# Kernel optimization log

Hardware: AMD Instinct MI355X
Metric: run time of the kernel (lower is better)

Reference implementation:

```python
import jax, jax.numpy as jnp
from jax import lax
import numpy as np

B, T, F = 256, 256, 40
H, A, HORIZON = 256, 64, 60
D_SP = 192


def setup_inputs() -> dict:
    key = jax.random.key(0)
    ks = jax.random.split(key, 16)
    s = 0.05  # weight scale to keep activations stable
    return {
        'x': jax.random.normal(ks[0], (B, T, F), jnp.float32),
        'W_sp': jax.random.normal(ks[1], (F, D_SP), jnp.float32) * s,
        'b_sp': jnp.zeros((D_SP,), jnp.float32),
        'Wx_ef': jax.random.normal(ks[2], (D_SP, 4 * H), jnp.float32) * s,
        'Wh_ef': jax.random.normal(ks[3], (H, 4 * H), jnp.float32) * s,
        'b_ef': jnp.zeros((4 * H,), jnp.float32),
        'Wx_eb': jax.random.normal(ks[4], (D_SP, 4 * H), jnp.float32) * s,
        'Wh_eb': jax.random.normal(ks[5], (H, 4 * H), jnp.float32) * s,
        'b_eb': jnp.zeros((4 * H,), jnp.float32),
        'We': jax.random.normal(ks[6], (2 * H, A), jnp.float32) * s,
        'Wd': jax.random.normal(ks[7], (H, A), jnp.float32) * s,
        'v': jax.random.normal(ks[8], (A,), jnp.float32) * s,
        'Wx_d': jax.random.normal(ks[9], (1 + 2 * H, 4 * H), jnp.float32) * s,
        'Wh_d': jax.random.normal(ks[10], (H, 4 * H), jnp.float32) * s,
        'b_d': jnp.zeros((4 * H,), jnp.float32),
        'W_ih': jax.random.normal(ks[11], (2 * H, H), jnp.float32) * s,
        'b_ih': jnp.zeros((H,), jnp.float32),
        'W_ic': jax.random.normal(ks[12], (2 * H, H), jnp.float32) * s,
        'b_ic': jnp.zeros((H,), jnp.float32),
        'Wo': jax.random.normal(ks[13], (H, 1), jnp.float32) * s,
        'bo': jnp.zeros((1,), jnp.float32),
    }


def _lstm_cell(x_t, h, c, Wx, Wh, b):
    g = x_t @ Wx + h @ Wh + b
    i, f, gg, o = jnp.split(g, 4, axis=-1)  # torch gate order i,f,g,o
    c = jax.nn.sigmoid(f) * c + jax.nn.sigmoid(i) * jnp.tanh(gg)
    h = jax.nn.sigmoid(o) * jnp.tanh(c)
    return h, c


def _lstm_scan(xs_tbd, Wx, Wh, b):
    # xs_tbd: [T, B, D] -> hs [T, B, H]
    h0 = jnp.zeros((xs_tbd.shape[1], Wh.shape[0]), xs_tbd.dtype)
    c0 = jnp.zeros_like(h0)
    def step(carry, x_t):
        h, c = carry
        h, c = _lstm_cell(x_t, h, c, Wx, Wh, b)
        return (h, c), h
    _, hs = lax.scan(step, (h0, c0), xs_tbd)
    return hs


def reference(x, W_sp, b_sp, Wx_ef, Wh_ef, b_ef, Wx_eb, Wh_eb, b_eb,
              We, Wd, v, Wx_d, Wh_d, b_d, W_ih, b_ih, W_ic, b_ic, Wo, bo):
    # spatial encoder (stand-in for DeepLOBEncoder): [B,T,F] -> [B,T,192]
    h_spatial = x @ W_sp + b_sp
    xs = jnp.swapaxes(h_spatial, 0, 1)          # [T, B, 192]
    hs_f = _lstm_scan(xs, Wx_ef, Wh_ef, b_ef)    # [T, B, H]
    hs_b = _lstm_scan(xs[::-1], Wx_eb, Wh_eb, b_eb)[::-1]
    enc_out = jnp.swapaxes(jnp.concatenate([hs_f, hs_b], axis=-1), 0, 1)  # [B,T,2H]

    enc_mean = enc_out.mean(axis=1)
    dec_h = jnp.tanh(enc_mean @ W_ih + b_ih)     # [B, H]
    dec_c = jnp.tanh(enc_mean @ W_ic + b_ic)

    enc_proj = enc_out @ We                      # [B, T, A] precomputed (same math)
    prev_y = ((x[:, -1, 0] + x[:, -1, 2]) / 2.0)[:, None]  # ask_idx=0, bid_idx=2

    def dec_step(carry, _):
        h, c, py = carry
        e = jnp.tanh(enc_proj + (h @ Wd)[:, None, :])        # [B,T,A]
        scores = e @ v                                        # [B,T]
        w = jax.nn.softmax(scores, axis=1)
        context = jnp.einsum('bt,bth->bh', w, enc_out)        # [B,2H]
        dec_in = jnp.concatenate([py, context], axis=1)       # [B,1+2H]
        h, c = _lstm_cell(dec_in, h, c, Wx_d, Wh_d, b_d)
        y = h @ Wo + bo                                       # [B,1]
        return (h, c, lax.stop_gradient(y)), y[:, 0]

    _, ys = lax.scan(dec_step, (dec_h, dec_c, prev_y), None, length=HORIZON)
    return jnp.swapaxes(ys, 0, 1)  # [B, horizon]
```

## Files before the change

kernel.cpp:

```cpp
#include <hip/hip_runtime.h>
#include <cmath>

#define B_ 256
#define T_ 256
#define F_ 40
#define H_ 256
#define A_ 64
#define HOR_ 60
#define DSP_ 192
#define ENC_NBLK 128
#define WSTR 456
#define FPAD 32
#define ADLD 1024
#define CT 56

typedef unsigned short u16;
typedef unsigned int u32;
typedef __attribute__((ext_vector_type(8))) short bf16x8;
typedef __attribute__((ext_vector_type(4))) float f32x4;
typedef __attribute__((ext_vector_type(8))) u32 u32x8;
typedef __attribute__((ext_vector_type(4))) u32 u32x4;

__device__ __forceinline__ float sigm(float x){ return 1.f/(1.f+expf(-x)); }

__device__ __forceinline__ u16 f2bf(float x){
  u32 u = __float_as_uint(x);
  u32 r = (u + 0x7FFFu + ((u>>16)&1u)) >> 16;
  return (u16)r;
}
__device__ __forceinline__ float bf2f(u16 h){ return __uint_as_float(((u32)h)<<16); }
__device__ __forceinline__ u32 packsplit(float x){
  u16 hi = f2bf(x);
  u16 lo = f2bf(x - bf2f(hi));
  return (u32)hi | ((u32)lo<<16);
}
__device__ __forceinline__ float unpack2f(u32 v){
  return __uint_as_float(v<<16) + __uint_as_float(v & 0xFFFF0000u);
}

__device__ __forceinline__ float wred_sum(float v){
  #pragma unroll
  for (int o=32;o>0;o>>=1) v += __shfl_xor(v,o);
  return v;
}
__device__ __forceinline__ float wred_max(float v){
  #pragma unroll
  for (int o=32;o>0;o>>=1) v = fmaxf(v,__shfl_xor(v,o));
  return v;
}

__device__ __forceinline__ void cnt_signal(int* c){
  __hip_atomic_fetch_add(c, 1, __ATOMIC_RELEASE, __HIP_MEMORY_SCOPE_AGENT);
}
template<int SLP>
__device__ __forceinline__ void cnt_wait4(const int* base, int need, int tid){
  if (tid < 4){
    const int* c = base + (size_t)tid*FPAD;
    while (__hip_atomic_load(c, __ATOMIC_ACQUIRE, __HIP_MEMORY_SCOPE_AGENT) < need)
      __builtin_amdgcn_s_sleep(SLP);
  }
  __syncthreads();
}

__global__ void conv_w(const float* __restrict__ Wx, const float* __restrict__ Wh,
                       u16* __restrict__ hi, u16* __restrict__ lo,
                       int KX, int Ktot, int N){
  int idx = blockIdx.x*256 + threadIdx.x;
  if (idx >= N*Ktot) return;
  int n = idx / Ktot, k = idx - n*Ktot;
  float w = (k < KX) ? Wx[(size_t)k*N + n] : Wh[(size_t)(k-KX)*N + n];
  u16 h = f2bf(w);
  hi[idx] = h;
  lo[idx] = f2bf(w - bf2f(h));
}

__global__ __launch_bounds__(192) void spatial_proj(
    const float* __restrict__ x, const float* __restrict__ W, const float* __restrict__ bsp,
    u32* __restrict__ hsp32){
  __shared__ float Ws[40][192];
  __shared__ float xr[40];
  int t = blockIdx.x, tid = threadIdx.x;
  for (int i = tid; i < 40*192; i += 192){ int k = i/192, c = i-k*192; Ws[k][c] = W[i]; }
  float bb = bsp[tid];
  __syncthreads();
  for (int b=0; b<B_; b++){
    if (tid < 40) xr[tid] = x[((size_t)b*T_ + t)*F_ + tid];
    __syncthreads();
    float acc = bb;
    #pragma unroll
    for (int k=0;k<40;k++) acc += xr[k]*Ws[k][tid];
    hsp32[((size_t)t*B_ + b)*DSP_ + tid] = packsplit(acc);
    __syncthreads();
  }
}

__global__ __launch_bounds__(256) void enc_scan(
    const u32* __restrict__ hsp32,
    const u16* __restrict__ W_hi, const u16* __restrict__ W_lo,
    const float* __restrict__ b_ef, const float* __restrict__ b_eb,
    u32* __restrict__ hbuf, u32* __restrict__ eo32, int* __restrict__ bar)
{
  extern __shared__ u16 smem[];
  u16* Whi = smem;
  u16* Wlo = smem + 4*16*WSTR;
  const int bid = blockIdx.x;
  const int grp = bid & 7;
  const int nt  = bid >> 3;
  const int dir = grp >> 2;
  const int m0  = (grp & 3) * 64;
  const int u0  = nt * 16;
  const int tid = threadIdx.x;
  const int wave = tid >> 6, lane = tid & 63;
  const int lrow = lane & 15, kblk = lane >> 4;
  const int koff = kblk * 8;
  {
    const size_t wbase = ((size_t)dir*1024 + u0) * 448;
    for (int idx = tid; idx < 4*16*448; idx += 256){
      int g = idx / (16*448);
      int r = idx - g*(16*448);
      int j = r / 448;
      int k = r - j*448;
      size_t go = wbase + ((size_t)g*256 + j)*448 + k;
      Whi[(g*16 + j)*WSTR + k] = W_hi[go];
      Wlo[(g*16 + j)*WSTR + k] = W_lo[go];
    }
  }
  const float* bias = dir ? b_eb : b_ef;
  float bg4[4];
  #pragma unroll
  for (int g=0; g<4; g++) bg4[g] = bias[g*H_ + u0 + lrow];
  __syncthreads();

  const int mrow = m0 + wave*16;
  const int arow = mrow + lrow;
  u32* hP0 = hbuf + (size_t)dir*(B_*H_);
  u32* hP1 = hbuf + (size_t)(2+dir)*(B_*H_);
  float c_reg[4] = {0.f,0.f,0.f,0.f};

  for (int s=0; s<T_; s++){
    const int t = dir ? (T_-1-s) : s;
    f32x4 acc[4] = {};
    const u32* abase = hsp32 + ((size_t)t*B_ + arow)*DSP_;
    #pragma unroll
    for (int ks=0; ks<6; ks++){
      int kb = ks*32 + koff;
      u32x8 la = *(const u32x8*)(abase + kb);
      bf16x8 ah, al;
      #pragma unroll
      for (int j=0;j<8;j++){ ah[j]=(short)(la[j]&0xFFFFu); al[j]=(short)(la[j]>>16); }
      #pragma unroll
      for (int g=0; g<4; g++){
        bf16x8 bh = *(const bf16x8*)(Whi + (g*16+lrow)*WSTR + kb);
        bf16x8 bl = *(const bf16x8*)(Wlo + (g*16+lrow)*WSTR + kb);
        acc[g] = __builtin_amdgcn_mfma_f32_16x16x32_bf16(ah, bh, acc[g], 0,0,0);
        acc[g] = __builtin_amdgcn_mfma_f32_16x16x32_bf16(ah, bl, acc[g], 0,0,0);
        acc[g] = __builtin_amdgcn_mfma_f32_16x16x32_bf16(al, bh, acc[g], 0,0,0);
      }
    }
    if (s > 0)
      cnt_wait4<8>(bar + (size_t)((grp*T_ + (s-1))*4)*FPAD, 4, tid);
    const u32* hin = (s & 1) ? hP1 : hP0;
    u32* hout      = (s & 1) ? hP0 : hP1;
    const u32* hbase = hin + (size_t)arow*H_;
    #pragma unroll
    for (int ks=0; ks<8; ks++){
      int kb = ks*32 + koff;
      u32x8 la = *(const u32x8*)(hbase + kb);
      bf16x8 ah, al;
      #pragma unroll
      for (int j=0;j<8;j++){ ah[j]=(short)(la[j]&0xFFFFu); al[j]=(short)(la[j]>>16); }
      #pragma unroll
      for (int g=0; g<4; g++){
        bf16x8 bh = *(const bf16x8*)(Whi + (g*16+lrow)*WSTR + 192 + kb);
        bf16x8 bl = *(const bf16x8*)(Wlo + (g*16+lrow)*WSTR + 192 + kb);
        acc[g] = __builtin_amdgcn_mfma_f32_16x16x32_bf16(ah, bh, acc[g], 0,0,0);
        acc[g] = __builtin_amdgcn_mfma_f32_16x16x32_bf16(ah, bl, acc[g], 0,0,0);
        acc[g] = __builtin_amdgcn_mfma_f32_16x16x32_bf16(al, bh, acc[g], 0,0,0);
      }
    }
    #pragma unroll
    for (int r=0; r<4; r++){
      int brow = mrow + kblk*4 + r;
      float gi = acc[0][r] + bg4[0];
      float gf = acc[1][r] + bg4[1];
      float gg = acc[2][r] + bg4[2];
      float go = acc[3][r] + bg4[3];
      float cn = sigm(gf)*c_reg[r] + sigm(gi)*tanhf(gg);
      float hn = sigm(go)*tanhf(cn);
      c_reg[r] = cn;
      u32 hp = packsplit(hn);
      hout[(size_t)brow*H_ + u0 + lrow] = hp;
      eo32[((size_t)brow*T_ + t)*512 + dir*H_ + u0 + lrow] = hp;
    }
    if (s == T_-1) break;
    __syncthreads();
    if (tid == 0)
      cnt_signal(bar + (size_t)((grp*T_ + s)*4 + (nt>>2))*FPAD);
  }
}

__global__ __launch_bounds__(512) void dec_scan(
    const u32* __restrict__ eo32,
    const u16* __restrict__ Wet_hi, const u16* __restrict__ Wet_lo,
    const float* __restrict__ W_ih, const float* __restrict__ b_ih,
    const float* __restrict__ W_ic, const float* __restrict__ b_ic,
    const float* __restrict__ x, float* __restrict__ ep,
    const float* __restrict__ Wd, const float* __restrict__ v,
    const float* __restrict__ Wo, const float* __restrict__ bo,
    const u16* __restrict__ W_hi, const u16* __restrict__ W_lo,
    const float* __restrict__ b_d, const float* __restrict__ Wx_d,
    float* __restrict__ hdp, float* __restrict__ cd,
    u32* __restrict__ Ad32, float* __restrict__ py,
    float* __restrict__ out, int* __restrict__ cntA, int* __restrict__ cntB)
{
  __shared__ float sh_h[256], sh_hwd[64], sh_v[64], sh_sc[256], sh_w[256];
  __shared__ float red8[8][64];
  __shared__ float sh_red[4], sh_red2[4];
  __shared__ float redc[8][512];
  __shared__ float gl[8][16][16];
  __shared__ float em_s[512];
  __shared__ u32 eoL[CT*512];
  const int b = blockIdx.x, tid = threadIdx.x;
  const int wave = tid >> 6, lane = tid & 63;
  const int bx = ((b & 7) << 1) | ((b >> 3) & 1);
  const int by = b >> 4;
  const int cr = tid >> 4, cu = tid & 15;
  float c_reg = 0.f;
  float bg0=0,bg1=0,bg2=0,bg3=0, w00=0,w01=0,w02=0,w03=0;
  if (tid < 256){
    int uu = bx*16 + cu;
    bg0 = b_d[uu];       bg1 = b_d[256+uu];
    bg2 = b_d[512+uu];   bg3 = b_d[768+uu];
    w00 = Wx_d[uu];      w01 = Wx_d[256+uu];
    w02 = Wx_d[512+uu];  w03 = Wx_d[768+uu];
  }
  {
    const u32* src = eo32 + (size_t)b*T_*512;
    for (int i = tid; i < CT*512/4; i += 512)
      ((u32x4*)eoL)[i] = *(const u32x4*)(src + (size_t)i*4);
  }
  {
    const int lrow = lane & 15, kblk = lane >> 4, koff = kblk*8;
    #pragma unroll
    for (int mi=0; mi<2; mi++){
      int mt = wave*2 + mi;
      f32x4 acc[4] = {};
      for (int ks=0; ks<16; ks++){
        int kb = ks*32 + koff;
        u32x8 ld = *(const u32x8*)(eo32 + ((size_t)b*T_ + mt*16 + lrow)*512 + kb);
        bf16x8 ah, al;
        #pragma unroll
        for (int j=0;j<8;j++){ ah[j]=(short)(ld[j]&0xFFFFu); al[j]=(short)(ld[j]>>16); }
        #pragma unroll
        for (int nf=0; nf<4; nf++){
          bf16x8 bh = *(const bf16x8*)(Wet_hi + (size_t)(nf*16+lrow)*512 + kb);
          bf16x8 bl = *(const bf16x8*)(Wet_lo + (size_t)(nf*16+lrow)*512 + kb);
          acc[nf] = __builtin_amdgcn_mfma_f32_16x16x32_bf16(ah, bh, acc[nf], 0,0,0);
          acc[nf] = __builtin_amdgcn_mfma_f32_16x16x32_bf16(ah, bl, acc[nf], 0,0,0);
          acc[nf] = __builtin_amdgcn_mfma_f32_16x16x32_bf16(al, bh, acc[nf], 0,0,0);
        }
      }
      #pragma unroll
      for (int nf=0; nf<4; nf++)
        #pragma unroll
        for (int r=0; r<4; r++)
          ep[((size_t)b*T_ + mt*16 + kblk*4 + r)*64 + nf*16 + lrow] = acc[nf][r];
    }
  }
  {
    float cacc[8] = {};
    const u32* eo = eo32 + (size_t)b*T_*512 + lane*8;
    #pragma unroll 8
    for (int tt=0; tt<32; tt++){
      int t = wave*32 + tt;
      u32x4 e0 = *(const u32x4*)(eo + (size_t)t*512);
      u32x4 e1 = *(const u32x4*)(eo + (size_t)t*512 + 4);
      #pragma unroll
      for (int j=0;j<4;j++){ cacc[j] += unpack2f(e0[j]); cacc[4+j] += unpack2f(e1[j]); }
    }
    #pragma unroll
    for (int j=0;j<8;j++) redc[wave][lane*8+j] = cacc[j];
    __syncthreads();
    if (tid < 256){
      float s0=0.f, s1=0.f;
      #pragma unroll
      for (int q=0;q<8;q++){ s0 += redc[q][tid]; s1 += redc[q][256+tid]; }
      em_s[tid] = s0*(1.f/T_); em_s[256+tid] = s1*(1.f/T_);
    }
    __syncthreads();
  }
  if (tid < 256){
    float ah = b_ih[tid], ac = b_ic[tid];
    for (int k=0;k<512;k++){
      float e = em_s[k];
      ah += e*W_ih[(size_t)k*256 + tid];
      ac += e*W_ic[(size_t)k*256 + tid];
    }
    float h0 = tanhf(ah), c0 = tanhf(ac);
    sh_h[tid] = h0;
    hdp[(size_t)b*H_ + tid] = h0;
    Ad32[(size_t)b*ADLD + 512 + tid] = packsplit(h0);
    cd[(size_t)b*H_ + tid] = c0;
  }
  if (tid == 0){
    size_t xb = ((size_t)b*T_ + 255)*F_;
    py[b] = (x[xb] + x[xb+2])*0.5f;
  }
  if (tid >= 448) sh_v[tid-448] = v[tid-448];
  __syncthreads();
  for (int s=0; s<=HOR_; s++){
    if (s > 0){
      cnt_wait4<16>(cntB + (size_t)(((s-1)*16 + by)*4)*FPAD, 4, tid);
      if (tid < 256) sh_h[tid] = hdp[(size_t)(s&1)*B_*H_ + (size_t)b*H_ + tid];
      __syncthreads();
      if (tid < 256){
        float p = sh_h[tid] * Wo[tid];
        p = wred_sum(p);
        if ((tid & 63) == 0) sh_red[tid>>6] = p;
      }
      __syncthreads();
      if (tid == 0){
        float y = sh_red[0]+sh_red[1]+sh_red[2]+sh_red[3] + bo[0];
        out[b*HOR_ + (s-1)] = y;
        py[b] = y;
      }
    }
    if (s == HOR_) break;
    {
      float ssum = 0.f;
      for (int j=wave*32; j<wave*32+32; j++) ssum += sh_h[j]*Wd[(size_t)j*A_ + lane];
      red8[wave][lane] = ssum;
      __syncthreads();
      if (tid < 64){
        float a = 0.f;
        #pragma unroll
        for (int q=0;q<8;q++) a += red8[q][tid];
        sh_hwd[tid] = a;
      }
    }
    __syncthreads();
    {
      int t = tid >> 1, aa = tid & 1;
      const float4* ep4 = (const float4*)(ep + ((size_t)(b*T_+t))*A_ + aa*32);
      float partial = 0.f;
      #pragma unroll
      for (int q=0;q<8;q++){
        float4 e4 = ep4[q];
        int a0 = aa*32 + q*4;
        partial += tanhf(e4.x + sh_hwd[a0+0]) * sh_v[a0+0];
        partial += tanhf(e4.y + sh_hwd[a0+1]) * sh_v[a0+1];
        partial += tanhf(e4.z + sh_hwd[a0+2]) * sh_v[a0+2];
        partial += tanhf(e4.w + sh_hwd[a0+3]) * sh_v[a0+3];
      }
      partial += __shfl_xor(partial, 1);
      if (aa == 0) sh_sc[t] = partial;
    }
    __syncthreads();
    if (tid < 256){
      float sc = sh_sc[tid];
      float m = wred_max(sc);
      if ((tid&63)==0) sh_red[tid>>6] = m;
      __syncthreads();
      m = fmaxf(fmaxf(sh_red[0],sh_red[1]), fmaxf(sh_red[2],sh_red[3]));
      float e = expf(sc - m);
      float su = wred_sum(e);
      if ((tid&63)==0) sh_red2[tid>>6] = su;
      __syncthreads();
      su = (sh_red2[0]+sh_red2[1])+(sh_red2[2]+sh_red2[3]);
      sh_w[tid] = e / su;
    } else { __syncthreads(); __syncthreads(); }
    __syncthreads();
    {
      float cacc[8] = {};
      const int t0 = wave*32, t1 = t0 + 32;
      const int tL = (t1 < CT) ? t1 : CT;
      for (int t=t0; t<tL; ++t){
        float wgt = sh_w[t];
        const u32* p = eoL + t*512 + lane*8;
        u32x4 e0 = *(const u32x4*)p;
        u32x4 e1 = *(const u32x4*)(p + 4);
        #pragma unroll
        for (int j=0;j<4;j++){
          cacc[j]   += wgt * unpack2f(e0[j]);
          cacc[4+j] += wgt * unpack2f(e1[j]);
        }
      }
      const u32* eo = eo32 + (size_t)b*T_*512 + lane*8;
      const int tG = (t0 > CT) ? t0 : CT;
      #pragma unroll 8
      for (int t=tG; t<t1; ++t){
        float wgt = sh_w[t];
        u32x4 e0 = *(const u32x4*)(eo + (size_t)t*512);
        u32x4 e1 = *(const u32x4*)(eo + (size_t)t*512 + 4);
        #pragma unroll
        for (int j=0;j<4;j++){
          cacc[j]   += wgt * unpack2f(e0[j]);
          cacc[4+j] += wgt * unpack2f(e1[j]);
        }
      }
      #pragma unroll
      for (int j=0;j<8;j++) redc[wave][lane*8+j] = cacc[j];
    }
    __syncthreads();
    if (tid < 256){
      float c0 = 0.f, c1 = 0.f;
      #pragma unroll
      for (int q=0;q<8;q++){ c0 += redc[q][tid]; c1 += redc[q][256+tid]; }
      Ad32[(size_t)b*ADLD + tid]       = packsplit(c0);
      Ad32[(size_t)b*ADLD + 256 + tid] = packsplit(c1);
    }
    __syncthreads();
    if (tid == 0)
      cnt_signal(cntA + (size_t)((s*16 + (b>>4))*4 + ((b&15)>>2))*FPAD);
    const int par = s & 1;
    const int gB = wave & 3, khB = wave >> 2;
    const int r16 = lane & 15, kb4 = lane >> 4;
    f32x4 accB = {0.f,0.f,0.f,0.f};
    const u32* arB = Ad32 + (size_t)(by*16 + r16)*ADLD;
    const u16* WHB = W_hi + (size_t)(gB*256 + bx*16 + r16)*768;
    const u16* WLB = W_lo + (size_t)(gB*256 + bx*16 + r16)*768;
    const bool pre = (khB == 1) && (s > 0);
    if (pre){
      for (int ks=16; ks<24; ks++){
        int kb = ks*32 + kb4*8;
        int kp = kb + (par<<8);
        u32x8 ld = *(const u32x8*)(arB + kp);
        bf16x8 ah, al;
        #pragma unroll
        for (int j=0;j<8;j++){ ah[j]=(short)(ld[j]&0xFFFFu); al[j]=(short)(ld[j]>>16); }
        bf16x8 bh = *(const bf16x8*)(WHB + kb);
        bf16x8 bl = *(const bf16x8*)(WLB + kb);
        accB = __builtin_amdgcn_mfma_f32_16x16x32_bf16(ah, bh, accB, 0,0,0);
        accB = __builtin_amdgcn_mfma_f32_16x16x32_bf16(ah, bl, accB, 0,0,0);
        accB = __builtin_amdgcn_mfma_f32_16x16x32_bf16(al, bh, accB, 0,0,0);
      }
    }
    cnt_wait4<16>(cntA + (size_t)((s*16 + by)*4)*FPAD, 4, tid);
    if (s == 0 && tid < 256)
      c_reg = cd[(size_t)(by*16 + cr)*H_ + bx*16 + cu];
    {
      const int ksBeg = khB ? 8 : 0;
      const int ksEnd = khB ? (pre ? 16 : 24) : 8;
      for (int ks=ksBeg; ks<ksEnd; ks++){
        int kb = ks*32 + kb4*8;
        int kp = (kb < 512) ? kb : (kb + (par<<8));
        u32x8 ld = *(const u32x8*)(arB + kp);
        bf16x8 ah, al;
        #pragma unroll
        for (int j=0;j<8;j++){ ah[j]=(short)(ld[j]&0xFFFFu); al[j]=(short)(ld[j]>>16); }
        bf16x8 bh = *(const bf16x8*)(WHB + kb);
        bf16x8 bl = *(const bf16x8*)(WLB + kb);
        accB = __builtin_amdgcn_mfma_f32_16x16x32_bf16(ah, bh, accB, 0,0,0);
        accB = __builtin_amdgcn_mfma_f32_16x16x32_bf16(ah, bl, accB, 0,0,0);
        accB = __builtin_amdgcn_mfma_f32_16x16x32_bf16(al, bh, accB, 0,0,0);
      }
      #pragma unroll
      for (int vv=0; vv<4; vv++) gl[wave][kb4*4+vv][r16] = accB[vv];
    }
    __syncthreads();
    if (tid < 256){
      float pyr = py[by*16 + cr];
      float gi = gl[0][cr][cu] + gl[4][cr][cu] + bg0 + pyr*w00;
      float gf = gl[1][cr][cu] + gl[5][cr][cu] + bg1 + pyr*w01;
      float gg = gl[2][cr][cu] + gl[6][cr][cu] + bg2 + pyr*w02;
      float go = gl[3][cr][cu] + gl[7][cr][cu] + bg3 + pyr*w03;
      float cn = sigm(gf)*c_reg + sigm(gi)*tanhf(gg);
      float hn = sigm(go)*tanhf(cn);
      c_reg = cn;
      size_t ridx = (size_t)(by*16+cr)*H_ + bx*16+cu;
      hdp[(size_t)((s+1)&1)*B_*H_ + ridx] = hn;
      Ad32[(size_t)(by*16+cr)*ADLD + 512 + (((s+1)&1)<<8) + bx*16+cu] = packsplit(hn);
    }
    __syncthreads();
    if (tid == 0)
      cnt_signal(cntB + (size_t)((s*16 + by)*4 + (bx>>2))*FPAD);
  }
}

extern "C" void kernel_launch(void* const* d_in, const int* in_sizes, int n_in,
                              void* d_out, int out_size, void* d_ws, size_t ws_size,
                              hipStream_t stream)
{
  const float* x    = (const float*)d_in[0];
  const float* W_sp = (const float*)d_in[1];
  const float* b_sp = (const float*)d_in[2];
  const float* Wx_ef= (const float*)d_in[3];
  const float* Wh_ef= (const float*)d_in[4];
  const float* b_ef = (const float*)d_in[5];
  const float* Wx_eb= (const float*)d_in[6];
  const float* Wh_eb= (const float*)d_in[7];
  const float* b_eb = (const float*)d_in[8];
  const float* We   = (const float*)d_in[9];
  const float* Wd   = (const float*)d_in[10];
  const float* v    = (const float*)d_in[11];
  const float* Wx_d = (const float*)d_in[12];
  const float* Wh_d = (const float*)d_in[13];
  const float* b_d  = (const float*)d_in[14];
  const float* W_ih = (const float*)d_in[15];
  const float* b_ih = (const float*)d_in[16];
  const float* W_ic = (const float*)d_in[17];
  const float* b_ic = (const float*)d_in[18];
  const float* Wo   = (const float*)d_in[19];
  const float* bo   = (const float*)d_in[20];
  float* out = (float*)d_out;

  char* base = (char*)d_ws;
  auto alloc = [&](size_t bytes)->char*{
    char* p = base; base += (bytes + 255) & ~(size_t)255; return p;
  };
  u16* Wenc_hi = (u16*)alloc((size_t)2*1024*448*2);
  u16* Wenc_lo = (u16*)alloc((size_t)2*1024*448*2);
  u16* Wdec_hi = (u16*)alloc((size_t)1024*768*2);
  u16* Wdec_lo = (u16*)alloc((size_t)1024*768*2);
  u16* Wet_hi  = (u16*)alloc((size_t)64*512*2);
  u16* Wet_lo  = (u16*)alloc((size_t)64*512*2);
  u32* hsp32   = (u32*)alloc((size_t)T_*B_*DSP_*4);
  u32* hbuf    = (u32*)alloc((size_t)2*2*B_*H_*4);
  u32* eo32    = (u32*)alloc((size_t)B_*T_*512*4);
  float* ep    = (float*)alloc((size_t)B_*T_*64*4);
  float* cd    = (float*)alloc((size_t)B_*H_*4);
  float* hdp   = (float*)alloc((size_t)2*B_*H_*4);
  u32* Ad32    = (u32*)alloc((size_t)B_*ADLD*4);
  float* pyb   = (float*)alloc((size_t)B_*4);
  int* bar     = (int*)alloc((size_t)8*T_*4*FPAD*4);
  int* cntA    = (int*)alloc((size_t)HOR_*16*4*FPAD*4);
  int* cntB    = (int*)alloc((size_t)HOR_*16*4*FPAD*4);
  if ((size_t)(base - (char*)d_ws) > ws_size) return;

  conv_w<<<dim3(1792),256,0,stream>>>(Wx_ef, Wh_ef, Wenc_hi, Wenc_lo, DSP_, 448, 1024);
  conv_w<<<dim3(1792),256,0,stream>>>(Wx_eb, Wh_eb, Wenc_hi+458752, Wenc_lo+458752, DSP_, 448, 1024);
  conv_w<<<dim3(3072),256,0,stream>>>(Wx_d+1024, Wh_d, Wdec_hi, Wdec_lo, 512, 768, 1024);
  conv_w<<<dim3(128),256,0,stream>>>(We, We, Wet_hi, Wet_lo, 512, 512, 64);

  spatial_proj<<<dim3(256),192,0,stream>>>(x, W_sp, b_sp, hsp32);

  hipMemsetAsync(hbuf, 0, (size_t)2*B_*H_*4, stream);
  hipMemsetAsync(bar, 0, (size_t)8*T_*4*FPAD*4, stream);
  hipMemsetAsync(cntA, 0, (size_t)HOR_*16*4*FPAD*4, stream);
  hipMemsetAsync(cntB, 0, (size_t)HOR_*16*4*FPAD*4, stream);

  enc_scan<<<dim3(ENC_NBLK), dim3(256), 2*4*16*WSTR*2, stream>>>(
      hsp32, Wenc_hi, Wenc_lo, b_ef, b_eb, hbuf, eo32, bar);

  dec_scan<<<dim3(256),512,0,stream>>>(
      eo32, Wet_hi, Wet_lo, W_ih, b_ih, W_ic, b_ic, x, ep,
      Wd, v, Wo, bo, Wdec_hi, Wdec_lo, b_d, Wx_d,
      hdp, cd, Ad32, pyb, out, cntA, cntB);
}
```

Baseline: 5.435 ms.

## Use XCC-local relaxed flag barriers when sync groups share one XCD

Each block records its XCC id in a per-group mask. When every block of a synchronization group turns out to sit on the same XCD, the code swaps the release/acquire atomic counters for per-block relaxed flags, and loads shared state with relaxed atomic loads instead of cached vector loads. The decoder block mapping is also remapped so row groups follow the round-robin XCD placement and are more likely to share an XCD. The aim is to cut cross-XCD coherence and barrier latency in the sequential scan steps. The cost is scalarised atomic loads in place of wide vector loads, and correctness now depends on same-XCD L2 coherence under relaxed ordering.

```diff
diff --git a/kernel.cpp b/kernel.cpp
--- a/kernel.cpp
+++ b/kernel.cpp
@@ -49,6 +49,19 @@
   return v;
 }
 
+__device__ __forceinline__ u32 get_xcc(){
+  u32 v;
+  asm("s_getreg_b32 %0, hwreg(HW_REG_XCC_ID, 0, 32)" : "=s"(v));
+  return v & 15u;
+}
+
+__device__ __forceinline__ u32 a_ld(const u32* p){
+  return __hip_atomic_load(p, __ATOMIC_RELAXED, __HIP_MEMORY_SCOPE_AGENT);
+}
+__device__ __forceinline__ float a_ldf(const float* p){
+  return __hip_atomic_load(p, __ATOMIC_RELAXED, __HIP_MEMORY_SCOPE_AGENT);
+}
+
 __device__ __forceinline__ void cnt_signal(int* c){
   __hip_atomic_fetch_add(c, 1, __ATOMIC_RELEASE, __HIP_MEMORY_SCOPE_AGENT);
 }
@@ -57,6 +70,17 @@
   if (tid < 4){
     const int* c = base + (size_t)tid*FPAD;
     while (__hip_atomic_load(c, __ATOMIC_ACQUIRE, __HIP_MEMORY_SCOPE_AGENT) < need)
+      __builtin_amdgcn_s_sleep(SLP);
+  }
+  __syncthreads();
+}
+__device__ __forceinline__ void flag_set(int* f){
+  __hip_atomic_store(f, 1, __ATOMIC_RELAXED, __HIP_MEMORY_SCOPE_AGENT);
+}
+template<int SLP>
+__device__ __forceinline__ void flag_wait16(const int* base, int tid){
+  if (tid < 16){
+    while (__hip_atomic_load(base + tid, __ATOMIC_RELAXED, __HIP_MEMORY_SCOPE_AGENT) == 0)
       __builtin_amdgcn_s_sleep(SLP);
   }
   __syncthreads();
@@ -98,9 +122,11 @@
     const u32* __restrict__ hsp32,
     const u16* __restrict__ W_hi, const u16* __restrict__ W_lo,
     const float* __restrict__ b_ef, const float* __restrict__ b_eb,
-    u32* __restrict__ hbuf, u32* __restrict__ eo32, int* __restrict__ bar)
+    u32* __restrict__ hbuf, u32* __restrict__ eo32, int* __restrict__ bar,
+    int* __restrict__ fbar, int* __restrict__ maskE)
 {
   extern __shared__ u16 smem[];
+  __shared__ int shFast;
   u16* Whi = smem;
   u16* Wlo = smem + 4*16*WSTR;
   const int bid = blockIdx.x;
@@ -125,6 +151,8 @@
       Wlo[(g*16 + j)*WSTR + k] = W_lo[go];
     }
   }
+  if (tid == 0)
+    __hip_atomic_fetch_or(&maskE[grp], 1 << get_xcc(), __ATOMIC_RELEASE, __HIP_MEMORY_SCOPE_AGENT);
   const float* bias = dir ? b_eb : b_ef;
   float bg4[4];
   #pragma unroll
@@ -136,6 +164,7 @@
   u32* hP0 = hbuf + (size_t)dir*(B_*H_);
   u32* hP1 = hbuf + (size_t)(2+dir)*(B_*H_);
   float c_reg[4] = {0.f,0.f,0.f,0.f};
+  bool fast = false;
 
   for (int s=0; s<T_; s++){
     const int t = dir ? (T_-1-s) : s;
@@ -157,15 +186,28 @@
         acc[g] = __builtin_amdgcn_mfma_f32_16x16x32_bf16(al, bh, acc[g], 0,0,0);
       }
     }
-    if (s > 0)
-      cnt_wait4<8>(bar + (size_t)((grp*T_ + (s-1))*4)*FPAD, 4, tid);
+    if (s > 0){
+      if (s >= 2 && fast)
+        flag_wait16<2>(fbar + (size_t)(grp*T_ + (s-1))*16, tid);
+      else
+        cnt_wait4<8>(bar + (size_t)((grp*T_ + (s-1))*4)*FPAD, 4, tid);
+      if (s == 1){
+        if (tid == 0)
+          shFast = (__popc((u32)__hip_atomic_load(&maskE[grp], __ATOMIC_RELAXED,
+                    __HIP_MEMORY_SCOPE_AGENT)) == 1) ? 1 : 0;
+        __syncthreads();
+        fast = (shFast != 0);
+      }
+    }
     const u32* hin = (s & 1) ? hP1 : hP0;
     u32* hout      = (s & 1) ? hP0 : hP1;
     const u32* hbase = hin + (size_t)arow*H_;
     #pragma unroll
     for (int ks=0; ks<8; ks++){
       int kb = ks*32 + koff;
-      u32x8 la = *(const u32x8*)(hbase + kb);
+      u32 la[8];
+      #pragma unroll
+      for (int j=0;j<8;j++) la[j] = a_ld(hbase + kb + j);
       bf16x8 ah, al;
       #pragma unroll
       for (int j=0;j<8;j++){ ah[j]=(short)(la[j]&0xFFFFu); al[j]=(short)(la[j]>>16); }
@@ -194,8 +236,12 @@
     }
     if (s == T_-1) break;
     __syncthreads();
-    if (tid == 0)
-      cnt_signal(bar + (size_t)((grp*T_ + s)*4 + (nt>>2))*FPAD);
+    if (tid == 0){
+      if (s >= 1 && fast)
+        flag_set(fbar + (size_t)(grp*T_ + s)*16 + nt);
+      else
+        cnt_signal(bar + (size_t)((grp*T_ + s)*4 + (nt>>2))*FPAD);
+    }
   }
 }
 
@@ -211,7 +257,8 @@
     const float* __restrict__ b_d, const float* __restrict__ Wx_d,
     float* __restrict__ hdp, float* __restrict__ cd,
     u32* __restrict__ Ad32, float* __restrict__ py,
-    float* __restrict__ out, int* __restrict__ cntA, int* __restrict__ cntB)
+    float* __restrict__ out, int* __restrict__ cntA, int* __restrict__ cntB,
+    int* __restrict__ fA, int* __restrict__ fB, int* __restrict__ maskD)
 {
   __shared__ float sh_h[256], sh_hwd[64], sh_v[64], sh_sc[256], sh_w[256];
   __shared__ float red8[8][64];
@@ -219,13 +266,17 @@
   __shared__ float redc[8][512];
   __shared__ float gl[8][16][16];
   __shared__ float em_s[512];
+  __shared__ int shFast;
   __shared__ u32 eoL[CT*512];
   const int b = blockIdx.x, tid = threadIdx.x;
   const int wave = tid >> 6, lane = tid & 63;
-  const int bx = ((b & 7) << 1) | ((b >> 3) & 1);
-  const int by = b >> 4;
+  const int q8 = b & 7, j32 = b >> 3;
+  const int by = 2*q8 + (j32 >> 4);
+  const int bx = j32 & 15;
+  const int row = by*16 + bx;
   const int cr = tid >> 4, cu = tid & 15;
   float c_reg = 0.f;
+  bool fastD = false;
   float bg0=0,bg1=0,bg2=0,bg3=0, w00=0,w01=0,w02=0,w03=0;
   if (tid < 256){
     int uu = bx*16 + cu;
@@ -235,7 +286,7 @@
     w02 = Wx_d[512+uu];  w03 = Wx_d[768+uu];
   }
   {
-    const u32* src = eo32 + (size_t)b*T_*512;
+    const u32* src = eo32 + (size_t)row*T_*512;
     for (int i = tid; i < CT*512/4; i += 512)
       ((u32x4*)eoL)[i] = *(const u32x4*)(src + (size_t)i*4);
   }
@@ -247,7 +298,7 @@
       f32x4 acc[4] = {};
       for (int ks=0; ks<16; ks++){
         int kb = ks*32 + koff;
-        u32x8 ld = *(const u32x8*)(eo32 + ((size_t)b*T_ + mt*16 + lrow)*512 + kb);
+        u32x8 ld = *(const u32x8*)(eo32 + ((size_t)row*T_ + mt*16 + lrow)*512 + kb);
         bf16x8 ah, al;
         #pragma unroll
         for (int j=0;j<8;j++){ ah[j]=(short)(ld[j]&0xFFFFu); al[j]=(short)(ld[j]>>16); }
@@ -264,12 +315,12 @@
       for (int nf=0; nf<4; nf++)
         #pragma unroll
         for (int r=0; r<4; r++)
-          ep[((size_t)b*T_ + mt*16 + kblk*4 + r)*64 + nf*16 + lrow] = acc[nf][r];
+          ep[((size_t)row*T_ + mt*16 + kblk*4 + r)*64 + nf*16 + lrow] = acc[nf][r];
     }
   }
   {
     float cacc[8] = {};
-    const u32* eo = eo32 + (size_t)b*T_*512 + lane*8;
+    const u32* eo = eo32 + (size_t)row*T_*512 + lane*8;
     #pragma unroll 8
     for (int tt=0; tt<32; tt++){
       int t = wave*32 + tt;
@@ -298,20 +349,22 @@
     }
     float h0 = tanhf(ah), c0 = tanhf(ac);
     sh_h[tid] = h0;
-    hdp[(size_t)b*H_ + tid] = h0;
-    Ad32[(size_t)b*ADLD + 512 + tid] = packsplit(h0);
-    cd[(size_t)b*H_ + tid] = c0;
+    hdp[(size_t)row*H_ + tid] = h0;
+    Ad32[(size_t)row*ADLD + 512 + tid] = packsplit(h0);
+    cd[(size_t)row*H_ + tid] = c0;
   }
   if (tid == 0){
-    size_t xb = ((size_t)b*T_ + 255)*F_;
-    py[b] = (x[xb] + x[xb+2])*0.5f;
+    size_t xb = ((size_t)row*T_ + 255)*F_;
+    py[row] = (x[xb] + x[xb+2])*0.5f;
+    __hip_atomic_fetch_or(&maskD[by], 1 << get_xcc(), __ATOMIC_RELEASE, __HIP_MEMORY_SCOPE_AGENT);
   }
   if (tid >= 448) sh_v[tid-448] = v[tid-448];
   __syncthreads();
   for (int s=0; s<=HOR_; s++){
     if (s > 0){
-      cnt_wait4<16>(cntB + (size_t)(((s-1)*16 + by)*4)*FPAD, 4, tid);
-      if (tid < 256) sh_h[tid] = hdp[(size_t)(s&1)*B_*H_ + (size_t)b*H_ + tid];
+      if (fastD) flag_wait16<4>(fB + (size_t)((s-1)*16 + by)*16, tid);
+      else       cnt_wait4<16>(cntB + (size_t)(((s-1)*16 + by)*4)*FPAD, 4, tid);
+      if (tid < 256) sh_h[tid] = a_ldf(hdp + (size_t)(s&1)*B_*H_ + (size_t)row*H_ + tid);
       __syncthreads();
       if (tid < 256){
         float p = sh_h[tid] * Wo[tid];
@@ -321,8 +374,8 @@
       __syncthreads();
       if (tid == 0){
         float y = sh_red[0]+sh_red[1]+sh_red[2]+sh_red[3] + bo[0];
-        out[b*HOR_ + (s-1)] = y;
-        py[b] = y;
+        out[row*HOR_ + (s-1)] = y;
+        py[row] = y;
       }
     }
     if (s == HOR_) break;
@@ -341,7 +394,7 @@
     __syncthreads();
     {
       int t = tid >> 1, aa = tid & 1;
-      const float4* ep4 = (const float4*)(ep + ((size_t)(b*T_+t))*A_ + aa*32);
+      const float4* ep4 = (const float4*)(ep + ((size_t)(row*T_+t))*A_ + aa*32);
       float partial = 0.f;
       #pragma unroll
       for (int q=0;q<8;q++){
@@ -385,7 +438,7 @@
           cacc[4+j] += wgt * unpack2f(e1[j]);
         }
       }
-      const u32* eo = eo32 + (size_t)b*T_*512 + lane*8;
+      const u32* eo = eo32 + (size_t)row*T_*512 + lane*8;
       const int tG = (t0 > CT) ? t0 : CT;
       #pragma unroll 8
       for (int t=tG; t<t1; ++t){
@@ -406,12 +459,14 @@
       float c0 = 0.f, c1 = 0.f;
       #pragma unroll
       for (int q=0;q<8;q++){ c0 += redc[q][tid]; c1 += redc[q][256+tid]; }
-      Ad32[(size_t)b*ADLD + tid]       = packsplit(c0);
-      Ad32[(size_t)b*ADLD + 256 + tid] = packsplit(c1);
-    }
-    __syncthreads();
-    if (tid == 0)
-      cnt_signal(cntA + (size_t)((s*16 + (b>>4))*4 + ((b&15)>>2))*FPAD);
+      Ad32[(size_t)row*ADLD + tid]       = packsplit(c0);
+      Ad32[(size_t)row*ADLD + 256 + tid] = packsplit(c1);
+    }
+    __syncthreads();
+    if (tid == 0){
+      if (s >= 1 && fastD) flag_set(fA + (size_t)(s*16 + by)*16 + bx);
+      else cnt_signal(cntA + (size_t)((s*16 + by)*4 + (bx>>2))*FPAD);
+    }
     const int par = s & 1;
     const int gB = wave & 3, khB = wave >> 2;
     const int r16 = lane & 15, kb4 = lane >> 4;
@@ -424,10 +479,12 @@
       for (int ks=16; ks<24; ks++){
         int kb = ks*32 + kb4*8;
         int kp = kb + (par<<8);
-        u32x8 ld = *(const u32x8*)(arB + kp);
+        u32 lv[8];
+        #pragma unroll
+        for (int j=0;j<8;j++) lv[j] = a_ld(arB + kp + j);
         bf16x8 ah, al;
         #pragma unroll
-        for (int j=0;j<8;j++){ ah[j]=(short)(ld[j]&0xFFFFu); al[j]=(short)(ld[j]>>16); }
+        for (int j=0;j<8;j++){ ah[j]=(short)(lv[j]&0xFFFFu); al[j]=(short)(lv[j]>>16); }
         bf16x8 bh = *(const bf16x8*)(WHB + kb);
         bf16x8 bl = *(const bf16x8*)(WLB + kb);
         accB = __builtin_amdgcn_mfma_f32_16x16x32_bf16(ah, bh, accB, 0,0,0);
@@ -435,19 +492,31 @@
         accB = __builtin_amdgcn_mfma_f32_16x16x32_bf16(al, bh, accB, 0,0,0);
       }
     }
-    cnt_wait4<16>(cntA + (size_t)((s*16 + by)*4)*FPAD, 4, tid);
-    if (s == 0 && tid < 256)
-      c_reg = cd[(size_t)(by*16 + cr)*H_ + bx*16 + cu];
+    if (s == 0 || !fastD)
+      cnt_wait4<16>(cntA + (size_t)((s*16 + by)*4)*FPAD, 4, tid);
+    else
+      flag_wait16<4>(fA + (size_t)(s*16 + by)*16, tid);
+    if (s == 0){
+      if (tid == 0)
+        shFast = (__popc((u32)__hip_atomic_load(&maskD[by], __ATOMIC_RELAXED,
+                  __HIP_MEMORY_SCOPE_AGENT)) == 1) ? 1 : 0;
+      __syncthreads();
+      fastD = (shFast != 0);
+      if (tid < 256)
+        c_reg = cd[(size_t)(by*16 + cr)*H_ + bx*16 + cu];
+    }
     {
       const int ksBeg = khB ? 8 : 0;
       const int ksEnd = khB ? (pre ? 16 : 24) : 8;
       for (int ks=ksBeg; ks<ksEnd; ks++){
         int kb = ks*32 + kb4*8;
         int kp = (kb < 512) ? kb : (kb + (par<<8));
-        u32x8 ld = *(const u32x8*)(arB + kp);
+        u32 lv[8];
+        #pragma unroll
+        for (int j=0;j<8;j++) lv[j] = a_ld(arB + kp + j);
         bf16x8 ah, al;
         #pragma unroll
-        for (int j=0;j<8;j++){ ah[j]=(short)(ld[j]&0xFFFFu); al[j]=(short)(ld[j]>>16); }
+        for (int j=0;j<8;j++){ ah[j]=(short)(lv[j]&0xFFFFu); al[j]=(short)(lv[j]>>16); }
         bf16x8 bh = *(const bf16x8*)(WHB + kb);
         bf16x8 bl = *(const bf16x8*)(WLB + kb);
         accB = __builtin_amdgcn_mfma_f32_16x16x32_bf16(ah, bh, accB, 0,0,0);
@@ -459,7 +528,7 @@
     }
     __syncthreads();
     if (tid < 256){
-      float pyr = py[by*16 + cr];
+      float pyr = a_ldf(py + by*16 + cr);
       float gi = gl[0][cr][cu] + gl[4][cr][cu] + bg0 + pyr*w00;
       float gf = gl[1][cr][cu] + gl[5][cr][cu] + bg1 + pyr*w01;
       float gg = gl[2][cr][cu] + gl[6][cr][cu] + bg2 + pyr*w02;
@@ -472,8 +541,10 @@
       Ad32[(size_t)(by*16+cr)*ADLD + 512 + (((s+1)&1)<<8) + bx*16+cu] = packsplit(hn);
     }
     __syncthreads();
-    if (tid == 0)
-      cnt_signal(cntB + (size_t)((s*16 + by)*4 + (bx>>2))*FPAD);
+    if (tid == 0){
+      if (fastD) flag_set(fB + (size_t)(s*16 + by)*16 + bx);
+      else cnt_signal(cntB + (size_t)((s*16 + by)*4 + (bx>>2))*FPAD);
+    }
   }
 }
 
@@ -525,6 +596,11 @@
   int* bar     = (int*)alloc((size_t)8*T_*4*FPAD*4);
   int* cntA    = (int*)alloc((size_t)HOR_*16*4*FPAD*4);
   int* cntB    = (int*)alloc((size_t)HOR_*16*4*FPAD*4);
+  int* fbarE   = (int*)alloc((size_t)8*T_*16*4);
+  int* fA      = (int*)alloc((size_t)HOR_*16*16*4);
+  int* fB      = (int*)alloc((size_t)HOR_*16*16*4);
+  int* maskE   = (int*)alloc((size_t)8*4);
+  int* maskD   = (int*)alloc((size_t)16*4);
   if ((size_t)(base - (char*)d_ws) > ws_size) return;
 
   conv_w<<<dim3(1792),256,0,stream>>>(Wx_ef, Wh_ef, Wenc_hi, Wenc_lo, DSP_, 448, 1024);
@@ -538,12 +614,17 @@
   hipMemsetAsync(bar, 0, (size_t)8*T_*4*FPAD*4, stream);
   hipMemsetAsync(cntA, 0, (size_t)HOR_*16*4*FPAD*4, stream);
   hipMemsetAsync(cntB, 0, (size_t)HOR_*16*4*FPAD*4, stream);
+  hipMemsetAsync(fbarE, 0, (size_t)8*T_*16*4, stream);
+  hipMemsetAsync(fA, 0, (size_t)HOR_*16*16*4, stream);
+  hipMemsetAsync(fB, 0, (size_t)HOR_*16*16*4, stream);
+  hipMemsetAsync(maskE, 0, (size_t)8*4, stream);
+  hipMemsetAsync(maskD, 0, (size_t)16*4, stream);
 
   enc_scan<<<dim3(ENC_NBLK), dim3(256), 2*4*16*WSTR*2, stream>>>(
-      hsp32, Wenc_hi, Wenc_lo, b_ef, b_eb, hbuf, eo32, bar);
+      hsp32, Wenc_hi, Wenc_lo, b_ef, b_eb, hbuf, eo32, bar, fbarE, maskE);
 
   dec_scan<<<dim3(256),512,0,stream>>>(
       eo32, Wet_hi, Wet_lo, W_ih, b_ih, W_ic, b_ic, x, ep,
       Wd, v, Wo, bo, Wdec_hi, Wdec_lo, b_d, Wx_d,
-      hdp, cd, Ad32, pyb, out, cntA, cntB);
-}
+      hdp, cd, Ad32, pyb, out, cntA, cntB, fA, fB, maskD);
+}
```

New measurement: 6.918 ms. 27.3% more time.
